# Optimization experiments

Measured on AMD Instinct MI355X. Metric: run time of the kernel, lower is better.

The kernel has to match this reference:

```python
import jax, jax.numpy as jnp
import numpy as np

N_NODES = 50000
N_EDGES = 1250000
D_IN = 64
D_HID = 64
D_OUT = 16
N_GRAPHS = 128


def setup_inputs() -> dict:
    key = jax.random.key(0)
    ks = jax.random.split(key, 16)
    glorot = lambda k, shape: jax.random.normal(k, shape, jnp.float32) * (2.0 / (shape[0] + shape[1])) ** 0.5
    inp = {
        "x": jax.random.normal(ks[0], (N_NODES, D_IN), jnp.float32),
        "edge_index": jax.random.randint(ks[1], (2, N_EDGES), 0, N_NODES, jnp.int32),
        "adj": jnp.zeros((1,), jnp.float32),
        "batch": jnp.sort(jax.random.randint(ks[2], (N_NODES,), 0, N_GRAPHS, jnp.int32)),
        # GraphConv layer 1: lin_rel (with bias) on aggregated msgs, lin_root (no bias) on x
        "W_rel1": glorot(ks[3], (D_IN, D_HID)),
        "b_rel1": jnp.zeros((D_HID,), jnp.float32),
        "W_root1": glorot(ks[4], (D_IN, D_HID)),
        "W_rel2": glorot(ks[5], (D_HID, D_HID)),
        "b_rel2": jnp.zeros((D_HID,), jnp.float32),
        "W_root2": glorot(ks[6], (D_HID, D_HID)),
        "W_rel3": glorot(ks[7], (D_HID, D_HID)),
        "b_rel3": jnp.zeros((D_HID,), jnp.float32),
        "W_root3": glorot(ks[8], (D_HID, D_HID)),
        "W_lin": glorot(ks[9], (D_HID, D_OUT)),
        "b_lin": jnp.zeros((D_OUT,), jnp.float32),
    }
    return inp


def graph_conv(x, src, dst, W_rel, b_rel, W_root):
    # PyG GraphConv (aggr='add'): out[i] = (sum_{j->i} x[j]) @ W_rel + b_rel + x[i] @ W_root
    agg = jax.ops.segment_sum(x[src], dst, num_segments=N_NODES)  # [N, d]
    return agg @ W_rel + b_rel + x @ W_root


def reference(x, edge_index, adj, batch,
              W_rel1, b_rel1, W_root1,
              W_rel2, b_rel2, W_root2,
              W_rel3, b_rel3, W_root3,
              W_lin, b_lin):
    src, dst = edge_index[0], edge_index[1]
    h = jax.nn.relu(graph_conv(x, src, dst, W_rel1, b_rel1, W_root1))
    h = jax.nn.relu(graph_conv(h, src, dst, W_rel2, b_rel2, W_root2))
    h = graph_conv(h, src, dst, W_rel3, b_rel3, W_root3)
    # global_mean_pool over batch ids
    sums = jax.ops.segment_sum(h, batch, num_segments=N_GRAPHS)  # [G, d]
    counts = jax.ops.segment_sum(jnp.ones((h.shape[0],), h.dtype), batch, num_segments=N_GRAPHS)
    pooled = sums / jnp.maximum(counts, 1.0)[:, None]
    return pooled @ W_lin + b_lin  # [G, D_OUT]
```

## Files before the change

kernel.cpp:

```cpp
#include <hip/hip_runtime.h>

#define D 64
#define N_GRAPHS 128
#define D_OUT 16
#define BCAP 16384
#define TILE 4096
#define ECAP 2048

typedef unsigned short u16;
typedef unsigned int u32;
typedef unsigned char u8;
typedef __attribute__((ext_vector_type(8))) short bf16x8;
typedef __attribute__((ext_vector_type(4))) float f32x4;
typedef __attribute__((ext_vector_type(2))) float f32x2;

__device__ inline u16 f2bf(float f) {
  u32 u = __float_as_uint(f);
  return (u16)((u + 0x7fffu + ((u >> 16) & 1u)) >> 16);
}
__device__ inline float bf2f(u16 b) { return __uint_as_float((u32)b << 16); }
__device__ inline f32x2 bfpair(u32 v) {
  return (f32x2){__uint_as_float(v << 16), __uint_as_float(v & 0xffff0000u)};
}

__global__ __launch_bounds__(256) void cvtbin_kernel(
    const float* __restrict__ xin, u16* __restrict__ hX, int n4, int nbin,
    const int* __restrict__ src, const int* __restrict__ dst,
    int* __restrict__ cursors, u32* __restrict__ binned, int n_edges, int nbuck,
    const float* __restrict__ Wrel1, const float* __restrict__ Wroot1,
    const float* __restrict__ Wrel2, const float* __restrict__ Wroot2,
    const float* __restrict__ Wrel3, const float* __restrict__ Wroot3,
    const float* __restrict__ Wlin, const float* __restrict__ brel3,
    const float* __restrict__ blin,
    float* __restrict__ M1, float* __restrict__ M2, float* __restrict__ cvec,
    u16* __restrict__ WbT1r, u16* __restrict__ WbT1o,
    u16* __restrict__ WbT2r, u16* __restrict__ WbT2o) {
  __shared__ u32 ent[TILE];
  __shared__ u8 ebk[TILE];
  __shared__ int hist[256];
  __shared__ int startb[256];
  __shared__ int cur[256];
  __shared__ int gbase[256];
  int t = threadIdx.x;

  if ((int)blockIdx.x < nbin) {
    hist[t] = 0;
    __syncthreads();
    int base = blockIdx.x * TILE;
    int cnt = n_edges - base;
    if (cnt > TILE) cnt = TILE;

    int mys[16], myd[16];
#pragma unroll
    for (int j = 0; j < 16; j++) {
      int i = base + t + j * 256;
      if (t + j * 256 < cnt) {
        mys[j] = src[i];
        myd[j] = dst[i];
        atomicAdd(&hist[myd[j] >> 8], 1);
      } else {
        myd[j] = -1;
      }
    }
    __syncthreads();
    int myc = hist[t];
    for (int off = 1; off < 256; off <<= 1) {
      int tmp = (t >= off) ? hist[t - off] : 0;
      __syncthreads();
      hist[t] += tmp;
      __syncthreads();
    }
    int excl = hist[t] - myc;
    startb[t] = excl;
    cur[t] = excl;
    __syncthreads();

#pragma unroll
    for (int j = 0; j < 16; j++) {
      if (myd[j] >= 0) {
        int b = myd[j] >> 8;
        int p = atomicAdd(&cur[b], 1);
        ent[p] = ((u32)myd[j] << 16) | (u32)mys[j];
        ebk[p] = (u8)b;
      }
    }
    __syncthreads();

    if (t < nbuck && myc > 0) gbase[t] = atomicAdd(&cursors[t], myc);
    __syncthreads();

#pragma unroll
    for (int j = 0; j < 16; j++) {
      int p = t + j * 256;
      if (p < cnt) {
        int b = ebk[p];
        int gpos = gbase[b] + (p - startb[b]);
        if (gpos < BCAP) binned[(size_t)b * BCAP + gpos] = ent[p];
      }
    }
    return;
  }

  int cb = blockIdx.x - nbin;
  if (cb == 0) {
    if (t >= 240) {
      int o = t - 240;
      float c = blin[o];
#pragma unroll
      for (int j = 0; j < D; j++) c = fmaf(brel3[j], Wlin[j * D_OUT + o], c);
      cvec[o] = c;
    }
  } else if (cb <= 8) {
    int idx = (cb - 1) * 256 + t;
    const float* W = (idx < 1024) ? Wrel3 : Wroot3;
    float* M = (idx < 1024) ? M1 : M2;
    int id = idx & 1023;
    int k = id >> 4, o = id & 15;
    float acc = 0.0f;
#pragma unroll
    for (int j = 0; j < D; j++) acc = fmaf(W[k * D + j], Wlin[j * D_OUT + o], acc);
    M[id] = acc;
  } else if (cb <= 16) {
    int tid = (cb - 9) * 256 + t;
    int mat = tid >> 9;
    int r = tid & 511;
    int o = r >> 3;
    int k0 = (r & 7) * 8;
    const float* Wsrc = (mat == 0) ? Wrel1 : (mat == 1) ? Wroot1
                       : (mat == 2) ? Wrel2 : Wroot2;
    u16* Wdst = (mat == 0) ? WbT1r : (mat == 1) ? WbT1o
               : (mat == 2) ? WbT2r : WbT2o;
    u16 tmp[8];
#pragma unroll
    for (int j = 0; j < 8; j++) tmp[j] = f2bf(Wsrc[(k0 + j) * D + o]);
    uint4 pw;
    pw.x = (u32)tmp[0] | ((u32)tmp[1] << 16);
    pw.y = (u32)tmp[2] | ((u32)tmp[3] << 16);
    pw.z = (u32)tmp[4] | ((u32)tmp[5] << 16);
    pw.w = (u32)tmp[6] | ((u32)tmp[7] << 16);
    *(uint4*)&Wdst[o * D + k0] = pw;
  }
  int i = cb * 256 + t;
  if (i >= n4) return;
  float4 v = ((const float4*)xin)[i];
  ushort4 o4;
  o4.x = f2bf(v.x); o4.y = f2bf(v.y); o4.z = f2bf(v.z); o4.w = f2bf(v.w);
  ((ushort4*)hX)[i] = o4;
}

__global__ __launch_bounds__(256) void csr_kernel(
    const u32* __restrict__ binned, const int* __restrict__ cursors,
    u16* __restrict__ csr_src, int* __restrict__ offsets,
    int n_nodes, int nbuck) {
  __shared__ int deg[256];
  __shared__ int cur[256];
  __shared__ int red[256];
  __shared__ u16 lcsr[BCAP];
  int b = blockIdx.x, t = threadIdx.x;
  int cnt = cursors[b];
  if (cnt < 0) cnt = 0;
  if (cnt > BCAP) cnt = BCAP;

  int c = 0;
  if (t < b) {
    c = cursors[t];
    if (c < 0) c = 0;
    if (c > BCAP) c = BCAP;
  }
  red[t] = c;
  __syncthreads();
  for (int off = 128; off > 0; off >>= 1) {
    if (t < off) red[t] += red[t + off];
    __syncthreads();
  }
  int ebase = red[0];

  int nodeBase = b << 8;
  int nn = n_nodes - nodeBase;
  if (nn > 256) nn = 256;

  deg[t] = 0;
  __syncthreads();
  const u32* be = binned + (size_t)b * BCAP;
  for (int i = t; i < cnt; i += 256)
    atomicAdd(&deg[(be[i] >> 16) - nodeBase], 1);
  __syncthreads();
  int myd = deg[t];
  for (int off = 1; off < 256; off <<= 1) {
    int tmp = (t >= off) ? deg[t - off] : 0;
    __syncthreads();
    deg[t] += tmp;
    __syncthreads();
  }
  int loff = deg[t] - myd;
  cur[t] = loff;
  if (t < nn) offsets[nodeBase + t] = ebase + loff;
  if (b == nbuck - 1 && t == 0) offsets[n_nodes] = ebase + cnt;
  __syncthreads();

  for (int i = t; i < cnt; i += 256) {
    u32 e = be[i];
    int ln = (e >> 16) - nodeBase;
    int p = atomicAdd(&cur[ln], 1);
    lcsr[p] = (u16)(e & 0xffffu);
  }
  __syncthreads();
  for (int i = t; i < cnt; i += 256) csr_src[ebase + i] = lcsr[i];
}

#define ACC8(a, r) \
  a[0] += bfpair(r.x); a[1] += bfpair(r.y); a[2] += bfpair(r.z); a[3] += bfpair(r.w);

#define GATHER_PROLOGUE(soff, permAr, eidx, blockBase, n_nodes, offsets, csr_src, gsrc, ebase0, scnt) \
  {                                                                     \
    int t_ = threadIdx.x;                                               \
    if (t_ < 33) {                                                      \
      int idx = blockBase + t_;                                         \
      if (idx > n_nodes) idx = n_nodes;                                 \
      soff[t_] = offsets[idx];                                          \
    }                                                                   \
    __syncthreads();                                                    \
    ebase0 = soff[0];                                                   \
    int ecnt_ = soff[32] - ebase0;                                      \
    scnt = ecnt_ < ECAP ? ecnt_ : ECAP;                                 \
    gsrc = csr_src + ebase0;                                            \
    if (t_ < 32) {                                                      \
      int d_ = (blockBase + t_ < n_nodes) ? soff[t_ + 1] - soff[t_] : -1; \
      int r_ = 0;                                                       \
      for (int j_ = 0; j_ < 32; j_++) {                                 \
        int dj_ = (blockBase + j_ < n_nodes) ? soff[j_ + 1] - soff[j_] : -1; \
        if (dj_ > d_ || (dj_ == d_ && j_ < t_)) r_++;                   \
      }                                                                 \
      permAr[r_] = (u8)t_;                                              \
    }                                                                   \
    for (int e_ = t_; e_ < scnt; e_ += 256) eidx[e_] = gsrc[e_];        \
    __syncthreads();                                                    \
  }

#define IDX(i) ((i) < ECAP ? (int)eidx[i] : (int)gsrc[i])

__global__ __launch_bounds__(256) void fused_layer_kernel(
    const u16* __restrict__ h, const int* __restrict__ offsets,
    const u16* __restrict__ csr_src,
    const u16* __restrict__ WbTrel, const u16* __restrict__ WbTroot,
    const float* __restrict__ brel,
    u16* __restrict__ h_out, int n_nodes, int do_relu) {
  __shared__ __align__(16) u16 ldsA[32 * 72];
  __shared__ __align__(16) u16 ldsX[32 * 72];
  __shared__ int soff[33];
  __shared__ u8 permAr[32];
  __shared__ u16 eidx[ECAP];
  int w = threadIdx.x >> 6;
  int lane = threadIdx.x & 63;
  int sub = lane >> 3;
  int fo = (lane & 7) * 8;
  int blockBase = blockIdx.x * 32;
  const u16* gsrc;
  int ebase0, scnt;

  GATHER_PROLOGUE(soff, permAr, eidx, blockBase, n_nodes, offsets, csr_src, gsrc, ebase0, scnt)

  int ln = permAr[w * 8 + sub];
  int node = blockBase + ln;
  bool valid = node < n_nodes;
  int ls = soff[ln] - ebase0;
  int le = soff[ln + 1] - ebase0;
  if (!valid) le = ls;
  int lrow = ln * 72;

  uint4 xr = make_uint4(0, 0, 0, 0);
  if (valid) xr = *(const uint4*)(h + ((size_t)node << 6) + fo);
  *(uint4*)&ldsX[lrow + fo] = xr;

  f32x2 a0[4] = {{0,0},{0,0},{0,0},{0,0}};
  f32x2 a1[4] = {{0,0},{0,0},{0,0},{0,0}};
  int i = ls;
  for (; i + 3 < le; i += 4) {
    int s0 = IDX(i), s1 = IDX(i + 1), s2 = IDX(i + 2), s3 = IDX(i + 3);
    uint4 r0 = *(const uint4*)(h + ((size_t)s0 << 6) + fo);
    uint4 r1 = *(const uint4*)(h + ((size_t)s1 << 6) + fo);
    uint4 r2 = *(const uint4*)(h + ((size_t)s2 << 6) + fo);
    uint4 r3 = *(const uint4*)(h + ((size_t)s3 << 6) + fo);
    ACC8(a0, r0) ACC8(a1, r1) ACC8(a0, r2) ACC8(a1, r3)
  }
  for (; i < le; i++) {
    int s0 = IDX(i);
    uint4 r0 = *(const uint4*)(h + ((size_t)s0 << 6) + fo);
    ACC8(a0, r0)
  }
#pragma unroll
  for (int k = 0; k < 4; k++) a0[k] += a1[k];

  uint4 pa;
  pa.x = (u32)f2bf(a0[0].x) | ((u32)f2bf(a0[0].y) << 16);
  pa.y = (u32)f2bf(a0[1].x) | ((u32)f2bf(a0[1].y) << 16);
  pa.z = (u32)f2bf(a0[2].x) | ((u32)f2bf(a0[2].y) << 16);
  pa.w = (u32)f2bf(a0[3].x) | ((u32)f2bf(a0[3].y) << 16);
  *(uint4*)&ldsA[lrow + fo] = pa;
  __syncthreads();

  int mt = w & 1;
  int ntb = (w >> 1) * 2;
  int lr = lane & 15, lk = lane >> 4;
  int arow = (mt * 16 + lr) * 72;
  bf16x8 af0 = *(const bf16x8*)&ldsA[arow + lk * 8];
  bf16x8 af1 = *(const bf16x8*)&ldsA[arow + 32 + lk * 8];
  bf16x8 xf0 = *(const bf16x8*)&ldsX[arow + lk * 8];
  bf16x8 xf1 = *(const bf16x8*)&ldsX[arow + 32 + lk * 8];
#pragma unroll
  for (int tt = 0; tt < 2; tt++) {
    int nt = ntb + tt;
    int wrow = (nt * 16 + lr) * D + lk * 8;
    bf16x8 br0 = *(const bf16x8*)(WbTrel + wrow);
    bf16x8 br1 = *(const bf16x8*)(WbTrel + wrow + 32);
    bf16x8 bo0 = *(const bf16x8*)(WbTroot + wrow);
    bf16x8 bo1 = *(const bf16x8*)(WbTroot + wrow + 32);
    f32x4 acc = {0.0f, 0.0f, 0.0f, 0.0f};
    acc = __builtin_amdgcn_mfma_f32_16x16x32_bf16(af0, br0, acc, 0, 0, 0);
    acc = __builtin_amdgcn_mfma_f32_16x16x32_bf16(af1, br1, acc, 0, 0, 0);
    acc = __builtin_amdgcn_mfma_f32_16x16x32_bf16(xf0, bo0, acc, 0, 0, 0);
    acc = __builtin_amdgcn_mfma_f32_16x16x32_bf16(xf1, bo1, acc, 0, 0, 0);
    float bias = brel[nt * 16 + lr];
#pragma unroll
    for (int r = 0; r < 4; r++) {
      int onode = blockBase + mt * 16 + lk * 4 + r;
      if (onode < n_nodes) {
        float v = acc[r] + bias;
        if (do_relu) v = fmaxf(v, 0.0f);
        h_out[((size_t)onode << 6) + nt * 16 + lr] = f2bf(v);
      }
    }
  }
}

__global__ __launch_bounds__(256) void gather_pool_kernel(
    const u16* __restrict__ h, const int* __restrict__ offsets,
    const u16* __restrict__ csr_src, const int* __restrict__ batch,
    float* __restrict__ pooledA, float* __restrict__ pooledH, int n_nodes) {
  __shared__ int soff[33];
  __shared__ u8 permAr[32];
  __shared__ u16 eidx[ECAP];
  __shared__ int gid[32];
  __shared__ float ldsPA[32][D];
  __shared__ float ldsPH[32][D];
  int w = threadIdx.x >> 6;
  int lane = threadIdx.x & 63;
  int sub = lane >> 3;
  int fo = (lane & 7) * 8;
  int blockBase = blockIdx.x * 32;
  if (threadIdx.x < 32)
    gid[threadIdx.x] = (blockBase + threadIdx.x < n_nodes) ? batch[blockBase + threadIdx.x] : -1;
  const u16* gsrc;
  int ebase0, scnt;

  GATHER_PROLOGUE(soff, permAr, eidx, blockBase, n_nodes, offsets, csr_src, gsrc, ebase0, scnt)

  int ln = permAr[w * 8 + sub];
  int node = blockBase + ln;
  bool valid = node < n_nodes;
  int ls = soff[ln] - ebase0;
  int le = soff[ln + 1] - ebase0;
  if (!valid) le = ls;

  f32x2 a0[4] = {{0,0},{0,0},{0,0},{0,0}};
  f32x2 a1[4] = {{0,0},{0,0},{0,0},{0,0}};
  int i = ls;
  for (; i + 3 < le; i += 4) {
    int s0 = IDX(i), s1 = IDX(i + 1), s2 = IDX(i + 2), s3 = IDX(i + 3);
    uint4 r0 = *(const uint4*)(h + ((size_t)s0 << 6) + fo);
    uint4 r1 = *(const uint4*)(h + ((size_t)s1 << 6) + fo);
    uint4 r2 = *(const uint4*)(h + ((size_t)s2 << 6) + fo);
    uint4 r3 = *(const uint4*)(h + ((size_t)s3 << 6) + fo);
    ACC8(a0, r0) ACC8(a1, r1) ACC8(a0, r2) ACC8(a1, r3)
  }
  for (; i < le; i++) {
    int s0 = IDX(i);
    uint4 r0 = *(const uint4*)(h + ((size_t)s0 << 6) + fo);
    ACC8(a0, r0)
  }
#pragma unroll
  for (int k = 0; k < 4; k++) a0[k] += a1[k];

  uint4 xr = make_uint4(0, 0, 0, 0);
  if (valid) xr = *(const uint4*)(h + ((size_t)node << 6) + fo);
  f32x2 x0 = bfpair(xr.x), x1 = bfpair(xr.y), x2 = bfpair(xr.z), x3 = bfpair(xr.w);
  float* rowA = &ldsPA[ln][fo];
  float* rowH = &ldsPH[ln][fo];
  rowA[0] = a0[0].x; rowA[1] = a0[0].y; rowA[2] = a0[1].x; rowA[3] = a0[1].y;
  rowA[4] = a0[2].x; rowA[5] = a0[2].y; rowA[6] = a0[3].x; rowA[7] = a0[3].y;
  rowH[0] = x0.x; rowH[1] = x0.y; rowH[2] = x1.x; rowH[3] = x1.y;
  rowH[4] = x2.x; rowH[5] = x2.y; rowH[6] = x3.x; rowH[7] = x3.y;
  __syncthreads();

  if (threadIdx.x < 128) {
    int half = threadIdx.x >> 6;
    int f = threadIdx.x & 63;
    float* dst = half ? pooledH : pooledA;
    float acc = 0.0f;
    int curg = -1;
#pragma unroll 1
    for (int n = 0; n < 32; n++) {
      int g = gid[n];
      if (g < 0) break;
      float v = half ? ldsPH[n][f] : ldsPA[n][f];
      if (g != curg) {
        if (curg >= 0) atomicAdd(dst + curg * D + f, acc);
        curg = g;
        acc = v;
      } else {
        acc += v;
      }
    }
    if (curg >= 0) atomicAdd(dst + curg * D + f, acc);
  }
}

__global__ __launch_bounds__(64) void final_kernel(
    const float* __restrict__ pooledA, const float* __restrict__ pooledH,
    const float* __restrict__ M1, const float* __restrict__ M2,
    const float* __restrict__ cvec, const float* __restrict__ blin,
    const int* __restrict__ batch, float* __restrict__ out, int n_nodes) {
  __shared__ int seg[2];
  int g = blockIdx.x;
  int t = threadIdx.x;
  if (t < 2) {
    int target = g + t;
    int lo = 0, hi = n_nodes;
    while (lo < hi) {
      int mid = (lo + hi) >> 1;
      if (batch[mid] < target) lo = mid + 1; else hi = mid;
    }
    seg[t] = lo;
  }
  __syncthreads();
  int cnt = seg[1] - seg[0];
  if (t < D_OUT) {
    float res;
    if (cnt > 0) {
      float inv = 1.0f / (float)cnt;
      float acc = cvec[t];
#pragma unroll
      for (int k = 0; k < D; k++)
        acc = fmaf(pooledA[g * D + k] * inv, M1[k * D_OUT + t],
              fmaf(pooledH[g * D + k] * inv, M2[k * D_OUT + t], acc));
      res = acc;
    } else {
      res = blin[t];
    }
    out[g * D_OUT + t] = res;
  }
}

extern "C" void kernel_launch(void* const* d_in, const int* in_sizes, int n_in,
                              void* d_out, int out_size, void* d_ws, size_t ws_size,
                              hipStream_t stream) {
  const float* x     = (const float*)d_in[0];
  const int*   ei    = (const int*)d_in[1];
  const int*   batch = (const int*)d_in[3];
  const float* Wrel1 = (const float*)d_in[4];
  const float* brel1 = (const float*)d_in[5];
  const float* Wroot1= (const float*)d_in[6];
  const float* Wrel2 = (const float*)d_in[7];
  const float* brel2 = (const float*)d_in[8];
  const float* Wroot2= (const float*)d_in[9];
  const float* Wrel3 = (const float*)d_in[10];
  const float* brel3 = (const float*)d_in[11];
  const float* Wroot3= (const float*)d_in[12];
  const float* Wlin  = (const float*)d_in[13];
  const float* blin  = (const float*)d_in[14];
  float* out = (float*)d_out;

  const int n_edges = in_sizes[1] / 2;
  const int n_nodes = in_sizes[0] / D;
  const int* src = ei;
  const int* dst = ei + n_edges;
  const int nbuck = (n_nodes + 255) >> 8;

  char* p = (char*)d_ws;
  u32* binned  = (u32*)p;    p += (size_t)nbuck * BCAP * sizeof(u32);
  int* cursors = (int*)p;    p += 256 * sizeof(int);
  float* pooledA = (float*)p; p += (size_t)N_GRAPHS * D * sizeof(float);
  float* pooledH = (float*)p; p += (size_t)N_GRAPHS * D * sizeof(float);
  float* M1     = (float*)p; p += (size_t)D * D_OUT * sizeof(float);
  float* M2     = (float*)p; p += (size_t)D * D_OUT * sizeof(float);
  float* cvec   = (float*)p; p += 16 * sizeof(float);
  int* offsets  = (int*)p;   p += (size_t)(n_nodes + 4) * sizeof(int);
  u16* hX       = (u16*)p;   p += (size_t)n_nodes * D * sizeof(u16);
  u16* h1       = (u16*)p;   p += (size_t)n_nodes * D * sizeof(u16);
  u16* h2       = (u16*)p;   p += (size_t)n_nodes * D * sizeof(u16);
  u16* csr_src  = (u16*)p;   p += (size_t)n_edges * sizeof(u16);
  u16* WbT1r    = (u16*)p;   p += (size_t)D * D * sizeof(u16);
  u16* WbT1o    = (u16*)p;   p += (size_t)D * D * sizeof(u16);
  u16* WbT2r    = (u16*)p;   p += (size_t)D * D * sizeof(u16);
  u16* WbT2o    = (u16*)p;   p += (size_t)D * D * sizeof(u16);

  const int bin_blocks = (n_edges + TILE - 1) / TILE;
  const int cvt_n4 = n_nodes * D / 4;
  const int cvt_blocks = (cvt_n4 + 255) / 256;
  const int fused_blocks = (n_nodes + 31) / 32;

  const size_t zero_bytes = 256 * sizeof(int) + 2 * (size_t)N_GRAPHS * D * sizeof(float);
  hipMemsetAsync(cursors, 0, zero_bytes, stream);

  cvtbin_kernel<<<bin_blocks + cvt_blocks, 256, 0, stream>>>(
      x, hX, cvt_n4, bin_blocks, src, dst, cursors, binned, n_edges, nbuck,
      Wrel1, Wroot1, Wrel2, Wroot2, Wrel3, Wroot3, Wlin, brel3, blin,
      M1, M2, cvec, WbT1r, WbT1o, WbT2r, WbT2o);
  csr_kernel<<<nbuck, 256, 0, stream>>>(binned, cursors, csr_src, offsets, n_nodes, nbuck);

  fused_layer_kernel<<<fused_blocks, 256, 0, stream>>>(
      hX, offsets, csr_src, WbT1r, WbT1o, brel1, h1, n_nodes, 1);
  fused_layer_kernel<<<fused_blocks, 256, 0, stream>>>(
      h1, offsets, csr_src, WbT2r, WbT2o, brel2, h2, n_nodes, 1);

  gather_pool_kernel<<<fused_blocks, 256, 0, stream>>>(
      h2, offsets, csr_src, batch, pooledA, pooledH, n_nodes);

  final_kernel<<<N_GRAPHS, 64, 0, stream>>>(
      pooledA, pooledH, M1, M2, cvec, blin, batch, out, n_nodes);
}
```

Baseline: 221.3 us.

## Merge layer, pooling and final kernels into one cooperative persistent kernel

```diff
diff --git a/kernel.cpp b/kernel.cpp
--- a/kernel.cpp
+++ b/kernel.cpp
@@ -1,4 +1,7 @@
 #include <hip/hip_runtime.h>
+#include <hip/hip_cooperative_groups.h>
+
+namespace cg = cooperative_groups;
 
 #define D 64
 #define N_GRAPHS 128
@@ -211,66 +214,80 @@
 #define ACC8(a, r) \
   a[0] += bfpair(r.x); a[1] += bfpair(r.y); a[2] += bfpair(r.z); a[3] += bfpair(r.w);
 
-#define GATHER_PROLOGUE(soff, permAr, eidx, blockBase, n_nodes, offsets, csr_src, gsrc, ebase0, scnt) \
-  {                                                                     \
-    int t_ = threadIdx.x;                                               \
-    if (t_ < 33) {                                                      \
-      int idx = blockBase + t_;                                         \
-      if (idx > n_nodes) idx = n_nodes;                                 \
-      soff[t_] = offsets[idx];                                          \
-    }                                                                   \
-    __syncthreads();                                                    \
-    ebase0 = soff[0];                                                   \
-    int ecnt_ = soff[32] - ebase0;                                      \
-    scnt = ecnt_ < ECAP ? ecnt_ : ECAP;                                 \
-    gsrc = csr_src + ebase0;                                            \
-    if (t_ < 32) {                                                      \
-      int d_ = (blockBase + t_ < n_nodes) ? soff[t_ + 1] - soff[t_] : -1; \
-      int r_ = 0;                                                       \
-      for (int j_ = 0; j_ < 32; j_++) {                                 \
-        int dj_ = (blockBase + j_ < n_nodes) ? soff[j_ + 1] - soff[j_] : -1; \
-        if (dj_ > d_ || (dj_ == d_ && j_ < t_)) r_++;                   \
-      }                                                                 \
-      permAr[r_] = (u8)t_;                                              \
-    }                                                                   \
-    for (int e_ = t_; e_ < scnt; e_ += 256) eidx[e_] = gsrc[e_];        \
-    __syncthreads();                                                    \
-  }
-
-#define IDX(i) ((i) < ECAP ? (int)eidx[i] : (int)gsrc[i])
-
-__global__ __launch_bounds__(256) void fused_layer_kernel(
-    const u16* __restrict__ h, const int* __restrict__ offsets,
-    const u16* __restrict__ csr_src,
+struct SmemT {
+  union {
+    struct { u16 A[32 * 72]; u16 X[32 * 72]; u16 eidx[ECAP]; } f;
+    struct { float PA[32][D]; float PH[32][D]; } p;
+  } u;
+  int soff[33];
+  u8 perm[32];
+  int gid[32];
+  int seg[2];
+};
+
+struct KArgs {
+  const u16* hX; u16* h1; u16* h2;
+  const int* offsets; const u16* csr; const int* batch;
+  const u16 *W1r, *W1o, *W2r, *W2o;
+  const float *b1, *b2;
+  float *pooledA, *pooledH;
+  const float *M1, *M2, *cvec, *blin;
+  float* out;
+  int n_nodes, nWork, phase_lo, phase_hi;
+};
+
+__device__ inline void gather_prologue(SmemT& sm, int blockBase, int n_nodes,
+                                       const int* __restrict__ offsets,
+                                       const u16* __restrict__ csr_src,
+                                       const u16*& gsrc, int& ebase0, int& scnt) {
+  int t = threadIdx.x;
+  if (t < 33) {
+    int idx = blockBase + t;
+    if (idx > n_nodes) idx = n_nodes;
+    sm.soff[t] = offsets[idx];
+  }
+  __syncthreads();
+  ebase0 = sm.soff[0];
+  int ecnt = sm.soff[32] - ebase0;
+  scnt = ecnt < ECAP ? ecnt : ECAP;
+  gsrc = csr_src + ebase0;
+  if (t < 32) {
+    int d_ = (blockBase + t < n_nodes) ? sm.soff[t + 1] - sm.soff[t] : -1;
+    int r_ = 0;
+    for (int j = 0; j < 32; j++) {
+      int dj = (blockBase + j < n_nodes) ? sm.soff[j + 1] - sm.soff[j] : -1;
+      if (dj > d_ || (dj == d_ && j < t)) r_++;
+    }
+    sm.perm[r_] = (u8)t;
+  }
+  for (int e = t; e < scnt; e += 256) sm.u.f.eidx[e] = gsrc[e];
+  __syncthreads();
+}
+
+#define IDX(i) ((i) < ECAP ? (int)sm.u.f.eidx[i] : (int)gsrc[i])
+
+__device__ void fused_work(SmemT& sm, int wb, const u16* __restrict__ h,
+    const int* __restrict__ offsets, const u16* __restrict__ csr_src,
     const u16* __restrict__ WbTrel, const u16* __restrict__ WbTroot,
-    const float* __restrict__ brel,
-    u16* __restrict__ h_out, int n_nodes, int do_relu) {
-  __shared__ __align__(16) u16 ldsA[32 * 72];
-  __shared__ __align__(16) u16 ldsX[32 * 72];
-  __shared__ int soff[33];
-  __shared__ u8 permAr[32];
-  __shared__ u16 eidx[ECAP];
-  int w = threadIdx.x >> 6;
-  int lane = threadIdx.x & 63;
-  int sub = lane >> 3;
-  int fo = (lane & 7) * 8;
-  int blockBase = blockIdx.x * 32;
-  const u16* gsrc;
-  int ebase0, scnt;
-
-  GATHER_PROLOGUE(soff, permAr, eidx, blockBase, n_nodes, offsets, csr_src, gsrc, ebase0, scnt)
-
-  int ln = permAr[w * 8 + sub];
+    const float* __restrict__ brel, u16* __restrict__ h_out,
+    int n_nodes, int do_relu) {
+  int t = threadIdx.x;
+  int w = t >> 6, lane = t & 63, sub = lane >> 3, fo = (lane & 7) * 8;
+  int blockBase = wb * 32;
+  const u16* gsrc; int ebase0, scnt;
+  gather_prologue(sm, blockBase, n_nodes, offsets, csr_src, gsrc, ebase0, scnt);
+
+  int ln = sm.perm[w * 8 + sub];
   int node = blockBase + ln;
   bool valid = node < n_nodes;
-  int ls = soff[ln] - ebase0;
-  int le = soff[ln + 1] - ebase0;
+  int ls = sm.soff[ln] - ebase0;
+  int le = sm.soff[ln + 1] - ebase0;
   if (!valid) le = ls;
   int lrow = ln * 72;
 
   uint4 xr = make_uint4(0, 0, 0, 0);
   if (valid) xr = *(const uint4*)(h + ((size_t)node << 6) + fo);
-  *(uint4*)&ldsX[lrow + fo] = xr;
+  *(uint4*)&sm.u.f.X[lrow + fo] = xr;
 
   f32x2 a0[4] = {{0,0},{0,0},{0,0},{0,0}};
   f32x2 a1[4] = {{0,0},{0,0},{0,0},{0,0}};
@@ -296,17 +313,17 @@
   pa.y = (u32)f2bf(a0[1].x) | ((u32)f2bf(a0[1].y) << 16);
   pa.z = (u32)f2bf(a0[2].x) | ((u32)f2bf(a0[2].y) << 16);
   pa.w = (u32)f2bf(a0[3].x) | ((u32)f2bf(a0[3].y) << 16);
-  *(uint4*)&ldsA[lrow + fo] = pa;
+  *(uint4*)&sm.u.f.A[lrow + fo] = pa;
   __syncthreads();
 
   int mt = w & 1;
   int ntb = (w >> 1) * 2;
   int lr = lane & 15, lk = lane >> 4;
   int arow = (mt * 16 + lr) * 72;
-  bf16x8 af0 = *(const bf16x8*)&ldsA[arow + lk * 8];
-  bf16x8 af1 = *(const bf16x8*)&ldsA[arow + 32 + lk * 8];
-  bf16x8 xf0 = *(const bf16x8*)&ldsX[arow + lk * 8];
-  bf16x8 xf1 = *(const bf16x8*)&ldsX[arow + 32 + lk * 8];
+  bf16x8 af0 = *(const bf16x8*)&sm.u.f.A[arow + lk * 8];
+  bf16x8 af1 = *(const bf16x8*)&sm.u.f.A[arow + 32 + lk * 8];
+  bf16x8 xf0 = *(const bf16x8*)&sm.u.f.X[arow + lk * 8];
+  bf16x8 xf1 = *(const bf16x8*)&sm.u.f.X[arow + 32 + lk * 8];
 #pragma unroll
   for (int tt = 0; tt < 2; tt++) {
     int nt = ntb + tt;
@@ -333,33 +350,23 @@
   }
 }
 
-__global__ __launch_bounds__(256) void gather_pool_kernel(
-    const u16* __restrict__ h, const int* __restrict__ offsets,
-    const u16* __restrict__ csr_src, const int* __restrict__ batch,
+__device__ void pool_work(SmemT& sm, int wb, const u16* __restrict__ h,
+    const int* __restrict__ offsets, const u16* __restrict__ csr_src,
+    const int* __restrict__ batch,
     float* __restrict__ pooledA, float* __restrict__ pooledH, int n_nodes) {
-  __shared__ int soff[33];
-  __shared__ u8 permAr[32];
-  __shared__ u16 eidx[ECAP];
-  __shared__ int gid[32];
-  __shared__ float ldsPA[32][D];
-  __shared__ float ldsPH[32][D];
-  int w = threadIdx.x >> 6;
-  int lane = threadIdx.x & 63;
-  int sub = lane >> 3;
-  int fo = (lane & 7) * 8;
-  int blockBase = blockIdx.x * 32;
-  if (threadIdx.x < 32)
-    gid[threadIdx.x] = (blockBase + threadIdx.x < n_nodes) ? batch[blockBase + threadIdx.x] : -1;
-  const u16* gsrc;
-  int ebase0, scnt;
-
-  GATHER_PROLOGUE(soff, permAr, eidx, blockBase, n_nodes, offsets, csr_src, gsrc, ebase0, scnt)
-
-  int ln = permAr[w * 8 + sub];
+  int t = threadIdx.x;
+  int w = t >> 6, lane = t & 63, sub = lane >> 3, fo = (lane & 7) * 8;
+  int blockBase = wb * 32;
+  if (t < 32)
+    sm.gid[t] = (blockBase + t < n_nodes) ? batch[blockBase + t] : -1;
+  const u16* gsrc; int ebase0, scnt;
+  gather_prologue(sm, blockBase, n_nodes, offsets, csr_src, gsrc, ebase0, scnt);
+
+  int ln = sm.perm[w * 8 + sub];
   int node = blockBase + ln;
   bool valid = node < n_nodes;
-  int ls = soff[ln] - ebase0;
-  int le = soff[ln + 1] - ebase0;
+  int ls = sm.soff[ln] - ebase0;
+  int le = sm.soff[ln + 1] - ebase0;
   if (!valid) le = ls;
 
   f32x2 a0[4] = {{0,0},{0,0},{0,0},{0,0}};
@@ -384,25 +391,27 @@
   uint4 xr = make_uint4(0, 0, 0, 0);
   if (valid) xr = *(const uint4*)(h + ((size_t)node << 6) + fo);
   f32x2 x0 = bfpair(xr.x), x1 = bfpair(xr.y), x2 = bfpair(xr.z), x3 = bfpair(xr.w);
-  float* rowA = &ldsPA[ln][fo];
-  float* rowH = &ldsPH[ln][fo];
+
+  __syncthreads();
+  float* rowA = &sm.u.p.PA[ln][fo];
+  float* rowH = &sm.u.p.PH[ln][fo];
   rowA[0] = a0[0].x; rowA[1] = a0[0].y; rowA[2] = a0[1].x; rowA[3] = a0[1].y;
   rowA[4] = a0[2].x; rowA[5] = a0[2].y; rowA[6] = a0[3].x; rowA[7] = a0[3].y;
   rowH[0] = x0.x; rowH[1] = x0.y; rowH[2] = x1.x; rowH[3] = x1.y;
   rowH[4] = x2.x; rowH[5] = x2.y; rowH[6] = x3.x; rowH[7] = x3.y;
   __syncthreads();
 
-  if (threadIdx.x < 128) {
-    int half = threadIdx.x >> 6;
-    int f = threadIdx.x & 63;
+  if (t < 128) {
+    int half = t >> 6;
+    int f = t & 63;
     float* dst = half ? pooledH : pooledA;
     float acc = 0.0f;
     int curg = -1;
 #pragma unroll 1
     for (int n = 0; n < 32; n++) {
-      int g = gid[n];
+      int g = sm.gid[n];
       if (g < 0) break;
-      float v = half ? ldsPH[n][f] : ldsPA[n][f];
+      float v = half ? sm.u.p.PH[n][f] : sm.u.p.PA[n][f];
       if (g != curg) {
         if (curg >= 0) atomicAdd(dst + curg * D + f, acc);
         curg = g;
@@ -415,13 +424,11 @@
   }
 }
 
-__global__ __launch_bounds__(64) void final_kernel(
+__device__ void final_work(SmemT& sm, int g,
     const float* __restrict__ pooledA, const float* __restrict__ pooledH,
     const float* __restrict__ M1, const float* __restrict__ M2,
     const float* __restrict__ cvec, const float* __restrict__ blin,
     const int* __restrict__ batch, float* __restrict__ out, int n_nodes) {
-  __shared__ int seg[2];
-  int g = blockIdx.x;
   int t = threadIdx.x;
   if (t < 2) {
     int target = g + t;
@@ -430,10 +437,10 @@
       int mid = (lo + hi) >> 1;
       if (batch[mid] < target) lo = mid + 1; else hi = mid;
     }
-    seg[t] = lo;
-  }
-  __syncthreads();
-  int cnt = seg[1] - seg[0];
+    sm.seg[t] = lo;
+  }
+  __syncthreads();
+  int cnt = sm.seg[1] - sm.seg[0];
   if (t < D_OUT) {
     float res;
     if (cnt > 0) {
@@ -448,6 +455,41 @@
       res = blin[t];
     }
     out[g * D_OUT + t] = res;
+  }
+}
+
+__global__ __launch_bounds__(256) void layers_kernel(KArgs a) {
+  __shared__ SmemT sm;
+  for (int ph = a.phase_lo; ph <= a.phase_hi; ++ph) {
+    if (ph == 0) {
+      for (int wb = blockIdx.x; wb < a.nWork; wb += gridDim.x) {
+        __syncthreads();
+        fused_work(sm, wb, a.hX, a.offsets, a.csr, a.W1r, a.W1o, a.b1, a.h1,
+                   a.n_nodes, 1);
+      }
+    } else if (ph == 1) {
+      for (int wb = blockIdx.x; wb < a.nWork; wb += gridDim.x) {
+        __syncthreads();
+        fused_work(sm, wb, a.h1, a.offsets, a.csr, a.W2r, a.W2o, a.b2, a.h2,
+                   a.n_nodes, 1);
+      }
+    } else if (ph == 2) {
+      for (int wb = blockIdx.x; wb < a.nWork; wb += gridDim.x) {
+        __syncthreads();
+        pool_work(sm, wb, a.h2, a.offsets, a.csr, a.batch,
+                  a.pooledA, a.pooledH, a.n_nodes);
+      }
+    } else {
+      for (int g = blockIdx.x; g < N_GRAPHS; g += gridDim.x) {
+        __syncthreads();
+        final_work(sm, g, a.pooledA, a.pooledH, a.M1, a.M2, a.cvec, a.blin,
+                   a.batch, a.out, a.n_nodes);
+      }
+    }
+    if (ph < a.phase_hi) {
+      __threadfence();
+      cg::this_grid().sync();
+    }
   }
 }
 
@@ -508,14 +550,32 @@
       M1, M2, cvec, WbT1r, WbT1o, WbT2r, WbT2o);
   csr_kernel<<<nbuck, 256, 0, stream>>>(binned, cursors, csr_src, offsets, n_nodes, nbuck);
 
-  fused_layer_kernel<<<fused_blocks, 256, 0, stream>>>(
-      hX, offsets, csr_src, WbT1r, WbT1o, brel1, h1, n_nodes, 1);
-  fused_layer_kernel<<<fused_blocks, 256, 0, stream>>>(
-      h1, offsets, csr_src, WbT2r, WbT2o, brel2, h2, n_nodes, 1);
-
-  gather_pool_kernel<<<fused_blocks, 256, 0, stream>>>(
-      h2, offsets, csr_src, batch, pooledA, pooledH, n_nodes);
-
-  final_kernel<<<N_GRAPHS, 64, 0, stream>>>(
-      pooledA, pooledH, M1, M2, cvec, blin, batch, out, n_nodes);
-}
+  KArgs ka;
+  ka.hX = hX; ka.h1 = h1; ka.h2 = h2;
+  ka.offsets = offsets; ka.csr = csr_src; ka.batch = batch;
+  ka.W1r = WbT1r; ka.W1o = WbT1o; ka.W2r = WbT2r; ka.W2o = WbT2o;
+  ka.b1 = brel1; ka.b2 = brel2;
+  ka.pooledA = pooledA; ka.pooledH = pooledH;
+  ka.M1 = M1; ka.M2 = M2; ka.cvec = cvec; ka.blin = blin;
+  ka.out = out;
+  ka.n_nodes = n_nodes; ka.nWork = fused_blocks;
+  ka.phase_lo = 0; ka.phase_hi = 3;
+
+  int maxPerCU = 0;
+  hipOccupancyMaxActiveBlocksPerMultiprocessor(&maxPerCU, layers_kernel, 256, 0);
+  bool coop = (maxPerCU > 0);
+  if (coop) {
+    int NB = maxPerCU * 256;
+    if (NB > fused_blocks) NB = fused_blocks;
+    void* kp[] = {&ka};
+    hipError_t e = hipLaunchCooperativeKernel((void*)layers_kernel,
+                                              dim3(NB), dim3(256), kp, 0, stream);
+    coop = (e == hipSuccess);
+  }
+  if (!coop) {
+    for (int ph = 0; ph < 4; ph++) {
+      ka.phase_lo = ka.phase_hi = ph;
+      layers_kernel<<<fused_blocks, 256, 0, stream>>>(ka);
+    }
+  }
+}
```

Result: slower. 535.0 us (+141.8%).
